# Optimization experiments

Measured on AMD Instinct MI355X. Metric: run time of the kernel, lower is better.

## Reference

```python
import jax, jax.numpy as jnp
import numpy as np

INPUT_DIM = 256
HIDDEN_DIM = 128
N = 16384


def setup_inputs() -> dict:
    key = jax.random.key(0)
    k_h, k_wq, k_bq, k_wk, k_bk = jax.random.split(key, 5)
    s = 1.0 / np.sqrt(INPUT_DIM)
    return {
        "H": jax.random.normal(k_h, (N, INPUT_DIM), dtype=jnp.float32),
        "Wq": jax.random.uniform(k_wq, (INPUT_DIM, HIDDEN_DIM), jnp.float32, -s, s),
        "bq": jax.random.uniform(k_bq, (HIDDEN_DIM,), jnp.float32, -s, s),
        "Wk": jax.random.uniform(k_wk, (INPUT_DIM, HIDDEN_DIM), jnp.float32, -s, s),
        "bk": jax.random.uniform(k_bk, (HIDDEN_DIM,), jnp.float32, -s, s),
    }


def reference(H, Wq, bq, Wk, bk):
    n = H.shape[0]
    Q = H @ Wq + bq                      # [N, hidden]
    K = H @ Wk + bk                      # [N, hidden]
    A = Q @ K.T                          # [N, N]
    # zero the diagonal BEFORE scaling/softmax (faithful to torch.where(eye,...))
    A = jnp.where(jnp.eye(n, dtype=bool), jnp.float32(0.0), A)
    A = A / jnp.sqrt(jnp.float32(K.shape[-1]))
    A = jax.nn.softmax(A, axis=-1)
    return A @ H + H                     # [N, T]
```

## Files before the change

### kernel.cpp

```cpp
#include <hip/hip_runtime.h>
#include <hip/hip_bf16.h>

#define NROWS 16384
#define DIN   256
#define DH    128
#define SPLITS 4
#define KVSPL  4096
#define KVBLK  64
#define NIT    (KVSPL / KVBLK)
#define QBLK   256

typedef __attribute__((ext_vector_type(8)))  short  short8;
typedef __attribute__((ext_vector_type(4)))  float  f32x4;
typedef __attribute__((ext_vector_type(16))) float  f32x16;
typedef __attribute__((ext_vector_type(4)))  unsigned short u16x4;
typedef __attribute__((ext_vector_type(4)))  unsigned int   u32x4;

__device__ __forceinline__ unsigned short f2bf(float f) {
  unsigned int u = __float_as_uint(f);
  unsigned int r = (u + 0x7FFFu + ((u >> 16) & 1u)) >> 16;
  return (unsigned short)r;
}
__device__ __forceinline__ float bf2f(unsigned short b) {
  return __uint_as_float(((unsigned int)b) << 16);
}

__device__ __forceinline__ void gload_lds16(const void* g, void* l) {
  __builtin_amdgcn_global_load_lds(
      (const __attribute__((address_space(1))) unsigned int*)g,
      (__attribute__((address_space(3))) unsigned int*)l, 16, 0, 0);
}

__global__ void prep_w(const float* __restrict__ Wq, const float* __restrict__ Wk,
                       unsigned short* __restrict__ WqT, unsigned short* __restrict__ WkT) {
  const float* W = blockIdx.x ? Wk : Wq;
  unsigned short* WT = blockIdx.x ? WkT : WqT;
  int c = threadIdx.x;
  for (int k = 0; k < DIN; ++k)
    WT[c * DIN + k] = f2bf(W[k * DH + c]);
}

__global__ __launch_bounds__(128) void prep_hqk(
    const float* __restrict__ H,
    const unsigned short* __restrict__ WqT, const float* __restrict__ bq,
    const unsigned short* __restrict__ WkT, const float* __restrict__ bk,
    unsigned short* __restrict__ HbT,
    unsigned short* __restrict__ Qb, unsigned short* __restrict__ Kb) {
  __shared__ __align__(16) unsigned short tile[32][264];
  const int tid = threadIdx.x;
  const int qbase = blockIdx.x * 32;

  for (int i = tid; i < 32 * 64; i += 128) {
    int r = i >> 6, c4 = i & 63;
    const f32x4 v = *reinterpret_cast<const f32x4*>(H + (size_t)(qbase + r) * DIN + c4 * 4);
    u16x4 b;
    b[0] = f2bf(v[0]); b[1] = f2bf(v[1]); b[2] = f2bf(v[2]); b[3] = f2bf(v[3]);
    *reinterpret_cast<u16x4*>(&tile[r][c4 * 4]) = b;
  }
  __syncthreads();

  for (int i = tid; i < 256 * 4; i += 128) {
    int c = i >> 2, seg = i & 3;
    short8 t;
#pragma unroll
    for (int j = 0; j < 8; ++j) t[j] = (short)tile[seg * 8 + j][c];
    *reinterpret_cast<short8*>(HbT + (size_t)c * NROWS + qbase + seg * 8) = t;
  }

  const int lane = tid & 63, w = tid >> 6;
  const int col = lane & 15, grp = lane >> 4;

  short8 ah[8];
#pragma unroll
  for (int c = 0; c < 8; ++c)
    ah[c] = *reinterpret_cast<const short8*>(&tile[w * 16 + col][c * 32 + grp * 8]);

  f32x4 accq[8], acck[8];
#pragma unroll
  for (int ct = 0; ct < 8; ++ct) { accq[ct] = f32x4{0,0,0,0}; acck[ct] = f32x4{0,0,0,0}; }

#pragma unroll
  for (int ct = 0; ct < 8; ++ct) {
#pragma unroll
    for (int c = 0; c < 8; ++c) {
      short8 bwq = *reinterpret_cast<const short8*>(WqT + (size_t)(ct * 16 + col) * DIN + c * 32 + grp * 8);
      accq[ct] = __builtin_amdgcn_mfma_f32_16x16x32_bf16(ah[c], bwq, accq[ct], 0, 0, 0);
      short8 bwk = *reinterpret_cast<const short8*>(WkT + (size_t)(ct * 16 + col) * DIN + c * 32 + grp * 8);
      acck[ct] = __builtin_amdgcn_mfma_f32_16x16x32_bf16(ah[c], bwk, acck[ct], 0, 0, 0);
    }
  }

  const float QSCALE = 0.12751742f;
#pragma unroll
  for (int ct = 0; ct < 8; ++ct) {
    float vbq = bq[ct * 16 + col];
    float vbk = bk[ct * 16 + col];
#pragma unroll
    for (int r = 0; r < 4; ++r) {
      int row = qbase + w * 16 + grp * 4 + r;
      Qb[(size_t)row * DH + ct * 16 + col] = f2bf((accq[ct][r] + vbq) * QSCALE);
      Kb[(size_t)row * DH + ct * 16 + col] = f2bf(acck[ct][r] + vbk);
    }
  }
}

__global__ __launch_bounds__(512, 2) void attn_fa(
    const unsigned short* __restrict__ Qb, const unsigned short* __restrict__ Kb,
    const unsigned short* __restrict__ HbT,
    unsigned short* __restrict__ Opart, float* __restrict__ Lp) {
  __shared__ __align__(16) char lds[99328];
  char* KtC = lds;
  char* VtC = lds + 32768;
  float* LsmF = (float*)(lds + 98304);

  const int tid = threadIdx.x;
  const int lane = tid & 63, w = tid >> 6;
  const int l31 = lane & 31, hi = lane >> 5;
  const int swz = (lane & 7) << 4;

  const int sp = blockIdx.x & 3;
  const int qb = blockIdx.x >> 2;
  const int qrow0 = qb * QBLK + w * 32;
  const int kv0 = sp * KVSPL;

  int koff[2];
#pragma unroll
  for (int s = 0; s < 2; ++s) {
    int kvl = (w * 2 + s) * 4 + (lane >> 4);
    int byt = (lane & 15) * 16;
    koff[s] = kvl * DH + ((byt ^ ((kvl & 7) << 4)) >> 1);
  }
  size_t voff[4];
#pragma unroll
  for (int s = 0; s < 4; ++s) {
    int d = (w * 4 + s) * 8 + (lane >> 3);
    int byt = (lane & 7) * 16;
    voff[s] = (size_t)d * NROWS + ((byt ^ ((d & 7) << 4)) >> 1);
  }

  short8 qf[8];
#pragma unroll
  for (int c = 0; c < 8; ++c)
    qf[c] = *reinterpret_cast<const short8*>(Qb + (size_t)(qrow0 + l31) * DH + c * 16 + hi * 8);

  f32x16 acc[8];
#pragma unroll
  for (int dt = 0; dt < 8; ++dt) acc[dt] = {};
  float lsum = 0.f;

  {
    const unsigned short* kbsrc = Kb + (size_t)kv0 * DH;
#pragma unroll
    for (int s = 0; s < 2; ++s)
      gload_lds16(kbsrc + koff[s], KtC + (w * 2 + s) * 1024);
#pragma unroll
    for (int s = 0; s < 4; ++s)
      gload_lds16(HbT + voff[s] + kv0, VtC + (w * 4 + s) * 1024);
  }

  const int dlv = l31 - 4 * hi;

  for (int it = 0; it < NIT; ++it) {
    const int pb = it & 1;
    char* Krd = KtC + pb * 16384;
    char* Vrd = VtC + pb * 32768;
    char* Kwr = KtC + (pb ^ 1) * 16384;
    char* Vwr = VtC + (pb ^ 1) * 32768;
    const int kvbase = kv0 + it * KVBLK;
    const int kvnext = kvbase + KVBLK;

    {
      const unsigned short* kbsrc = Kb + (size_t)kvnext * DH;
#pragma unroll
      for (int s = 0; s < 2; ++s)
        gload_lds16(kbsrc + koff[s], Kwr + (w * 2 + s) * 1024);
#pragma unroll
      for (int s = 0; s < 4; ++s)
        gload_lds16(HbT + voff[s] + kvnext, Vwr + (w * 4 + s) * 1024);
    }

    asm volatile("s_waitcnt vmcnt(6)" ::: "memory");
    __builtin_amdgcn_s_barrier();
    __builtin_amdgcn_sched_barrier(0);

    f32x16 p0 = {}, p1 = {};
#pragma unroll
    for (int c = 0; c < 8; ++c) {
      const int off = (c * 32 + hi * 16) ^ swz;
      short8 ka0 = *reinterpret_cast<const short8*>(Krd + l31 * 256 + off);
      short8 ka1 = *reinterpret_cast<const short8*>(Krd + 8192 + l31 * 256 + off);
      p0 = __builtin_amdgcn_mfma_f32_32x32x16_bf16(ka0, qf[c], p0, 0, 0, 0);
      p1 = __builtin_amdgcn_mfma_f32_32x32x16_bf16(ka1, qf[c], p1, 0, 0, 0);
    }

    const unsigned dq = (unsigned)(qrow0 - kvbase);
    if (dq < 64u) {
      if (dq == 0) {
#pragma unroll
        for (int r = 0; r < 16; ++r)
          if (dlv == ((r & 3) + 8 * (r >> 2))) p0[r] = 0.f;
      } else {
#pragma unroll
        for (int r = 0; r < 16; ++r)
          if (dlv == ((r & 3) + 8 * (r >> 2))) p1[r] = 0.f;
      }
    }

#pragma unroll
    for (int r = 0; r < 16; ++r) { p0[r] = exp2f(p0[r]); lsum += p0[r]; }
#pragma unroll
    for (int r = 0; r < 16; ++r) { p1[r] = exp2f(p1[r]); lsum += p1[r]; }

    unsigned int W[16];
#pragma unroll
    for (int j = 0; j < 8; ++j) {
      asm("v_cvt_pk_bf16_f32 %0, %1, %2" : "=v"(W[j])     : "v"(p0[2*j]), "v"(p0[2*j+1]));
      asm("v_cvt_pk_bf16_f32 %0, %1, %2" : "=v"(W[8 + j]) : "v"(p1[2*j]), "v"(p1[2*j+1]));
    }
#pragma unroll
    for (int b = 0; b < 4; ++b) {
      asm("v_permlane32_swap_b32 %0, %1" : "+v"(W[b*4+0]), "+v"(W[b*4+2]));
      asm("v_permlane32_swap_b32 %0, %1" : "+v"(W[b*4+1]), "+v"(W[b*4+3]));
    }

#pragma unroll
    for (int kc = 0; kc < 4; ++kc) {
      u32x4 paw = { W[kc*4+0], W[kc*4+1], W[kc*4+2], W[kc*4+3] };
      short8 pa = __builtin_bit_cast(short8, paw);
      const int off = (kc * 32 + hi * 16) ^ swz;
#pragma unroll
      for (int dt = 0; dt < 8; ++dt) {
        short8 bv = *reinterpret_cast<const short8*>(Vrd + (dt * 32 + l31) * 128 + off);
        acc[dt] = __builtin_amdgcn_mfma_f32_32x32x16_bf16(pa, bv, acc[dt], 0, 0, 0);
      }
    }

    __builtin_amdgcn_sched_barrier(0);
    __builtin_amdgcn_s_barrier();
  }

  lsum += __shfl_xor(lsum, 32);
  if (lane < 32) LsmF[w * 32 + l31] = lsum;
  asm volatile("s_waitcnt lgkmcnt(0)" ::: "memory");
  __builtin_amdgcn_sched_barrier(0);

  float rl[16];
#pragma unroll
  for (int r = 0; r < 16; ++r)
    rl[r] = 1.0f / LsmF[w * 32 + ((r & 3) + 8 * (r >> 2) + 4 * hi)];

  const size_t obase = (size_t)sp * NROWS * DIN;
#pragma unroll
  for (int dt = 0; dt < 8; ++dt) {
#pragma unroll
    for (int r = 0; r < 16; ++r) {
      int q = qrow0 + (r & 3) + 8 * (r >> 2) + 4 * hi;
      Opart[obase + (size_t)q * DIN + dt * 32 + l31] = f2bf(acc[dt][r] * rl[r]);
    }
  }
  if (lane < 32) Lp[(size_t)sp * NROWS + qrow0 + l31] = lsum;
}

__global__ __launch_bounds__(256) void merge_split(
    const unsigned short* __restrict__ Opart, const float* __restrict__ Lp,
    const float* __restrict__ H, float* __restrict__ out) {
  const int row = blockIdx.x * 16 + (threadIdx.x >> 4);
  const int d0 = (threadIdx.x & 15) * 16;

  float ls[SPLITS], Wt = 0.f;
#pragma unroll
  for (int s = 0; s < SPLITS; ++s) {
    ls[s] = Lp[(size_t)s * NROWS + row];
    Wt += ls[s];
  }
  float invW = 1.0f / Wt;

  float acc[16];
#pragma unroll
  for (int j = 0; j < 16; ++j) acc[j] = 0.f;
#pragma unroll
  for (int s = 0; s < SPLITS; ++s) {
    const unsigned short* p = Opart + ((size_t)s * NROWS + row) * DIN + d0;
#pragma unroll
    for (int h = 0; h < 2; ++h) {
      short8 v = *reinterpret_cast<const short8*>(p + h * 8);
#pragma unroll
      for (int j = 0; j < 8; ++j) acc[h * 8 + j] += ls[s] * bf2f((unsigned short)v[j]);
    }
  }
  const float* hrow = H + (size_t)row * DIN + d0;
  float* orow = out + (size_t)row * DIN + d0;
#pragma unroll
  for (int q = 0; q < 4; ++q) {
    f32x4 hv = *reinterpret_cast<const f32x4*>(hrow + q * 4);
    f32x4 ov;
#pragma unroll
    for (int j = 0; j < 4; ++j) ov[j] = acc[q * 4 + j] * invW + hv[j];
    *reinterpret_cast<f32x4*>(orow + q * 4) = ov;
  }
}

extern "C" void kernel_launch(void* const* d_in, const int* in_sizes, int n_in,
                              void* d_out, int out_size, void* d_ws, size_t ws_size,
                              hipStream_t stream) {
  const float* H  = (const float*)d_in[0];
  const float* Wq = (const float*)d_in[1];
  const float* bq = (const float*)d_in[2];
  const float* Wk = (const float*)d_in[3];
  const float* bk = (const float*)d_in[4];
  float* out = (float*)d_out;

  char* ws = (char*)d_ws;
  unsigned short* HbT   = (unsigned short*)(ws);
  unsigned short* Qb    = (unsigned short*)(ws + 8388608);
  unsigned short* Kb    = (unsigned short*)(ws + 12582912);
  unsigned short* WqT   = (unsigned short*)(ws + 16777216);
  unsigned short* WkT   = (unsigned short*)(ws + 16842752);
  unsigned short* Opart = (unsigned short*)(ws + 20971520);
  float*          Lp    = (float*)(ws + 54525952);

  prep_w<<<2, 128, 0, stream>>>(Wq, Wk, WqT, WkT);
  prep_hqk<<<512, 128, 0, stream>>>(H, WqT, bq, WkT, bk, HbT, Qb, Kb);
  attn_fa<<<256, 512, 0, stream>>>(Qb, Kb, HbT, Opart, Lp);
  merge_split<<<1024, 256, 0, stream>>>(Opart, Lp, H, out);
}
```

Measured before the change: 318.7 us.

## Load K straight to registers, 4-stage V ring, restage prep stores, drop per-split normalization

The attention kernel no longer stages K through LDS. Each wave now loads its K fragments directly from global memory into registers, and LDS becomes a 4-deep ring of V tiles with a new swizzle, with s_setprio set around the MFMA sections. The partial outputs are stored unnormalized, so the merge kernel just sums them and divides by the total sum, removing the per-split reciprocal and LDS round trip. The prep kernel doubles its rows per block and writes Q/K through LDS as coalesced 16-byte rows. The direct K loads depend on cache hits from every wave, and storing unnormalized bf16 partials changes rounding.

```diff
diff --git a/kernel.cpp b/kernel.cpp
--- a/kernel.cpp
+++ b/kernel.cpp
@@ -7,7 +7,7 @@
 #define SPLITS 4
 #define KVSPL  4096
 #define KVBLK  64
-#define NIT    (KVSPL / KVBLK)
+#define NIT    64
 #define QBLK   256
 
 typedef __attribute__((ext_vector_type(8)))  short  short8;
@@ -40,17 +40,17 @@
     WT[c * DIN + k] = f2bf(W[k * DH + c]);
 }
 
-__global__ __launch_bounds__(128) void prep_hqk(
+__global__ __launch_bounds__(256) void prep_hqk(
     const float* __restrict__ H,
     const unsigned short* __restrict__ WqT, const float* __restrict__ bq,
     const unsigned short* __restrict__ WkT, const float* __restrict__ bk,
     unsigned short* __restrict__ HbT,
     unsigned short* __restrict__ Qb, unsigned short* __restrict__ Kb) {
-  __shared__ __align__(16) unsigned short tile[32][264];
+  __shared__ __align__(16) unsigned short tile[64][264];
   const int tid = threadIdx.x;
-  const int qbase = blockIdx.x * 32;
-
-  for (int i = tid; i < 32 * 64; i += 128) {
+  const int qbase = blockIdx.x * 64;
+
+  for (int i = tid; i < 64 * 64; i += 256) {
     int r = i >> 6, c4 = i & 63;
     const f32x4 v = *reinterpret_cast<const f32x4*>(H + (size_t)(qbase + r) * DIN + c4 * 4);
     u16x4 b;
@@ -59,8 +59,8 @@
   }
   __syncthreads();
 
-  for (int i = tid; i < 256 * 4; i += 128) {
-    int c = i >> 2, seg = i & 3;
+  for (int i = tid; i < 256 * 8; i += 256) {
+    int c = i >> 3, seg = i & 7;
     short8 t;
 #pragma unroll
     for (int j = 0; j < 8; ++j) t[j] = (short)tile[seg * 8 + j][c];
@@ -91,16 +91,33 @@
   }
 
   const float QSCALE = 0.12751742f;
-#pragma unroll
-  for (int ct = 0; ct < 8; ++ct) {
-    float vbq = bq[ct * 16 + col];
-    float vbk = bk[ct * 16 + col];
-#pragma unroll
-    for (int r = 0; r < 4; ++r) {
-      int row = qbase + w * 16 + grp * 4 + r;
-      Qb[(size_t)row * DH + ct * 16 + col] = f2bf((accq[ct][r] + vbq) * QSCALE);
-      Kb[(size_t)row * DH + ct * 16 + col] = f2bf(acck[ct][r] + vbk);
-    }
+  float vbq[8], vbk[8];
+#pragma unroll
+  for (int ct = 0; ct < 8; ++ct) { vbq[ct] = bq[ct * 16 + col]; vbk[ct] = bk[ct * 16 + col]; }
+
+  __syncthreads();
+#pragma unroll
+  for (int ct = 0; ct < 8; ++ct)
+#pragma unroll
+    for (int r = 0; r < 4; ++r)
+      tile[w * 16 + grp * 4 + r][ct * 16 + col] = f2bf((accq[ct][r] + vbq[ct]) * QSCALE);
+  __syncthreads();
+  for (int i = tid; i < 1024; i += 256) {
+    int r = i >> 4, seg = i & 15;
+    *reinterpret_cast<short8*>(Qb + (size_t)(qbase + r) * DH + seg * 8) =
+        *reinterpret_cast<const short8*>(&tile[r][seg * 8]);
+  }
+  __syncthreads();
+#pragma unroll
+  for (int ct = 0; ct < 8; ++ct)
+#pragma unroll
+    for (int r = 0; r < 4; ++r)
+      tile[w * 16 + grp * 4 + r][ct * 16 + col] = f2bf(acck[ct][r] + vbk[ct]);
+  __syncthreads();
+  for (int i = tid; i < 1024; i += 256) {
+    int r = i >> 4, seg = i & 15;
+    *reinterpret_cast<short8*>(Kb + (size_t)(qbase + r) * DH + seg * 8) =
+        *reinterpret_cast<const short8*>(&tile[r][seg * 8]);
   }
 }
 
@@ -108,35 +125,26 @@
     const unsigned short* __restrict__ Qb, const unsigned short* __restrict__ Kb,
     const unsigned short* __restrict__ HbT,
     unsigned short* __restrict__ Opart, float* __restrict__ Lp) {
-  __shared__ __align__(16) char lds[99328];
-  char* KtC = lds;
-  char* VtC = lds + 32768;
-  float* LsmF = (float*)(lds + 98304);
+  __shared__ __align__(16) char lds[131072];
 
   const int tid = threadIdx.x;
   const int lane = tid & 63, w = tid >> 6;
   const int l31 = lane & 31, hi = lane >> 5;
-  const int swz = (lane & 7) << 4;
+  const int vswz = (l31 & 7) << 4;
+  const int dlv = l31 - 4 * hi;
 
   const int sp = blockIdx.x & 3;
   const int qb = blockIdx.x >> 2;
   const int qrow0 = qb * QBLK + w * 32;
   const int kv0 = sp * KVSPL;
 
-  int koff[2];
-#pragma unroll
-  for (int s = 0; s < 2; ++s) {
-    int kvl = (w * 2 + s) * 4 + (lane >> 4);
-    int byt = (lane & 15) * 16;
-    koff[s] = kvl * DH + ((byt ^ ((kvl & 7) << 4)) >> 1);
-  }
   size_t voff[4];
 #pragma unroll
   for (int s = 0; s < 4; ++s) {
-    int d = (w * 4 + s) * 8 + (lane >> 3);
-    int byt = (lane & 7) * 16;
-    voff[s] = (size_t)d * NROWS + ((byt ^ ((d & 7) << 4)) >> 1);
-  }
+    int d = w * 32 + s * 8 + (lane >> 3);
+    voff[s] = (size_t)d * NROWS + (((((lane & 7) * 16) ^ ((lane >> 3) << 4))) >> 1);
+  }
+  const int vdst = w * 4096;
 
   short8 qf[8];
 #pragma unroll
@@ -148,106 +156,93 @@
   for (int dt = 0; dt < 8; ++dt) acc[dt] = {};
   float lsum = 0.f;
 
-  {
-    const unsigned short* kbsrc = Kb + (size_t)kv0 * DH;
-#pragma unroll
-    for (int s = 0; s < 2; ++s)
-      gload_lds16(kbsrc + koff[s], KtC + (w * 2 + s) * 1024);
-#pragma unroll
-    for (int s = 0; s < 4; ++s)
-      gload_lds16(HbT + voff[s] + kv0, VtC + (w * 4 + s) * 1024);
-  }
-
-  const int dlv = l31 - 4 * hi;
-
-  for (int it = 0; it < NIT; ++it) {
-    const int pb = it & 1;
-    char* Krd = KtC + pb * 16384;
-    char* Vrd = VtC + pb * 32768;
-    char* Kwr = KtC + (pb ^ 1) * 16384;
-    char* Vwr = VtC + (pb ^ 1) * 32768;
-    const int kvbase = kv0 + it * KVBLK;
-    const int kvnext = kvbase + KVBLK;
-
-    {
-      const unsigned short* kbsrc = Kb + (size_t)kvnext * DH;
-#pragma unroll
-      for (int s = 0; s < 2; ++s)
-        gload_lds16(kbsrc + koff[s], Kwr + (w * 2 + s) * 1024);
-#pragma unroll
-      for (int s = 0; s < 4; ++s)
-        gload_lds16(HbT + voff[s] + kvnext, Vwr + (w * 4 + s) * 1024);
+#pragma unroll
+  for (int s = 0; s < 4; ++s)
+    gload_lds16(HbT + voff[s] + kv0, lds + vdst + s * 1024);
+
+  for (int ot = 0; ot < NIT / 4; ++ot) {
+#pragma unroll
+    for (int pz = 0; pz < 4; ++pz) {
+      const int it = ot * 4 + pz;
+      const int kvbase = kv0 + it * KVBLK;
+      const char* Vrd = lds + pz * 32768;
+      char* Vwr = lds + ((pz + 1) & 3) * 32768;
+
+      const unsigned short* kA = Kb + (size_t)(kvbase + l31) * DH + hi * 8;
+      const unsigned short* kB = Kb + (size_t)(kvbase + 32 + l31) * DH + hi * 8;
+      short8 ka0[8], ka1[8];
+#pragma unroll
+      for (int c = 0; c < 8; ++c) {
+        ka0[c] = *reinterpret_cast<const short8*>(kA + c * 16);
+        ka1[c] = *reinterpret_cast<const short8*>(kB + c * 16);
+      }
+
+      {
+        const size_t kvn = (size_t)kvbase + KVBLK;
+#pragma unroll
+        for (int s = 0; s < 4; ++s)
+          gload_lds16(HbT + voff[s] + kvn, Vwr + vdst + s * 1024);
+      }
+
+      asm volatile("s_waitcnt vmcnt(20)" ::: "memory");
+      __builtin_amdgcn_s_barrier();
+
+      f32x16 p0 = {}, p1 = {};
+      __builtin_amdgcn_s_setprio(1);
+#pragma unroll
+      for (int c = 0; c < 8; ++c) {
+        p0 = __builtin_amdgcn_mfma_f32_32x32x16_bf16(ka0[c], qf[c], p0, 0, 0, 0);
+        p1 = __builtin_amdgcn_mfma_f32_32x32x16_bf16(ka1[c], qf[c], p1, 0, 0, 0);
+      }
+      __builtin_amdgcn_s_setprio(0);
+
+      const unsigned dq = (unsigned)(qrow0 - kvbase);
+      if (dq < 64u) {
+        if (dq == 0) {
+#pragma unroll
+          for (int r = 0; r < 16; ++r)
+            if (dlv == ((r & 3) + 8 * (r >> 2))) p0[r] = 0.f;
+        } else {
+#pragma unroll
+          for (int r = 0; r < 16; ++r)
+            if (dlv == ((r & 3) + 8 * (r >> 2))) p1[r] = 0.f;
+        }
+      }
+
+#pragma unroll
+      for (int r = 0; r < 16; ++r) { p0[r] = exp2f(p0[r]); lsum += p0[r]; }
+#pragma unroll
+      for (int r = 0; r < 16; ++r) { p1[r] = exp2f(p1[r]); lsum += p1[r]; }
+
+      unsigned int W[16];
+#pragma unroll
+      for (int j = 0; j < 8; ++j) {
+        asm("v_cvt_pk_bf16_f32 %0, %1, %2" : "=v"(W[j])     : "v"(p0[2*j]), "v"(p0[2*j+1]));
+        asm("v_cvt_pk_bf16_f32 %0, %1, %2" : "=v"(W[8 + j]) : "v"(p1[2*j]), "v"(p1[2*j+1]));
+      }
+#pragma unroll
+      for (int b = 0; b < 4; ++b) {
+        asm("v_permlane32_swap_b32 %0, %1" : "+v"(W[b*4+0]), "+v"(W[b*4+2]));
+        asm("v_permlane32_swap_b32 %0, %1" : "+v"(W[b*4+1]), "+v"(W[b*4+3]));
+      }
+
+      __builtin_amdgcn_s_setprio(1);
+#pragma unroll
+      for (int kc = 0; kc < 4; ++kc) {
+        u32x4 paw = { W[kc*4+0], W[kc*4+1], W[kc*4+2], W[kc*4+3] };
+        short8 pa = __builtin_bit_cast(short8, paw);
+        const int off = (kc * 32 + hi * 16) ^ vswz;
+#pragma unroll
+        for (int dt = 0; dt < 8; ++dt) {
+          short8 bv = *reinterpret_cast<const short8*>(Vrd + (dt * 32 + l31) * 128 + off);
+          acc[dt] = __builtin_amdgcn_mfma_f32_32x32x16_bf16(pa, bv, acc[dt], 0, 0, 0);
+        }
+      }
+      __builtin_amdgcn_s_setprio(0);
     }
-
-    asm volatile("s_waitcnt vmcnt(6)" ::: "memory");
-    __builtin_amdgcn_s_barrier();
-    __builtin_amdgcn_sched_barrier(0);
-
-    f32x16 p0 = {}, p1 = {};
-#pragma unroll
-    for (int c = 0; c < 8; ++c) {
-      const int off = (c * 32 + hi * 16) ^ swz;
-      short8 ka0 = *reinterpret_cast<const short8*>(Krd + l31 * 256 + off);
-      short8 ka1 = *reinterpret_cast<const short8*>(Krd + 8192 + l31 * 256 + off);
-      p0 = __builtin_amdgcn_mfma_f32_32x32x16_bf16(ka0, qf[c], p0, 0, 0, 0);
-      p1 = __builtin_amdgcn_mfma_f32_32x32x16_bf16(ka1, qf[c], p1, 0, 0, 0);
-    }
-
-    const unsigned dq = (unsigned)(qrow0 - kvbase);
-    if (dq < 64u) {
-      if (dq == 0) {
-#pragma unroll
-        for (int r = 0; r < 16; ++r)
-          if (dlv == ((r & 3) + 8 * (r >> 2))) p0[r] = 0.f;
-      } else {
-#pragma unroll
-        for (int r = 0; r < 16; ++r)
-          if (dlv == ((r & 3) + 8 * (r >> 2))) p1[r] = 0.f;
-      }
-    }
-
-#pragma unroll
-    for (int r = 0; r < 16; ++r) { p0[r] = exp2f(p0[r]); lsum += p0[r]; }
-#pragma unroll
-    for (int r = 0; r < 16; ++r) { p1[r] = exp2f(p1[r]); lsum += p1[r]; }
-
-    unsigned int W[16];
-#pragma unroll
-    for (int j = 0; j < 8; ++j) {
-      asm("v_cvt_pk_bf16_f32 %0, %1, %2" : "=v"(W[j])     : "v"(p0[2*j]), "v"(p0[2*j+1]));
-      asm("v_cvt_pk_bf16_f32 %0, %1, %2" : "=v"(W[8 + j]) : "v"(p1[2*j]), "v"(p1[2*j+1]));
-    }
-#pragma unroll
-    for (int b = 0; b < 4; ++b) {
-      asm("v_permlane32_swap_b32 %0, %1" : "+v"(W[b*4+0]), "+v"(W[b*4+2]));
-      asm("v_permlane32_swap_b32 %0, %1" : "+v"(W[b*4+1]), "+v"(W[b*4+3]));
-    }
-
-#pragma unroll
-    for (int kc = 0; kc < 4; ++kc) {
-      u32x4 paw = { W[kc*4+0], W[kc*4+1], W[kc*4+2], W[kc*4+3] };
-      short8 pa = __builtin_bit_cast(short8, paw);
-      const int off = (kc * 32 + hi * 16) ^ swz;
-#pragma unroll
-      for (int dt = 0; dt < 8; ++dt) {
-        short8 bv = *reinterpret_cast<const short8*>(Vrd + (dt * 32 + l31) * 128 + off);
-        acc[dt] = __builtin_amdgcn_mfma_f32_32x32x16_bf16(pa, bv, acc[dt], 0, 0, 0);
-      }
-    }
-
-    __builtin_amdgcn_sched_barrier(0);
-    __builtin_amdgcn_s_barrier();
   }
 
   lsum += __shfl_xor(lsum, 32);
-  if (lane < 32) LsmF[w * 32 + l31] = lsum;
-  asm volatile("s_waitcnt lgkmcnt(0)" ::: "memory");
-  __builtin_amdgcn_sched_barrier(0);
-
-  float rl[16];
-#pragma unroll
-  for (int r = 0; r < 16; ++r)
-    rl[r] = 1.0f / LsmF[w * 32 + ((r & 3) + 8 * (r >> 2) + 4 * hi)];
 
   const size_t obase = (size_t)sp * NROWS * DIN;
 #pragma unroll
@@ -255,7 +250,7 @@
 #pragma unroll
     for (int r = 0; r < 16; ++r) {
       int q = qrow0 + (r & 3) + 8 * (r >> 2) + 4 * hi;
-      Opart[obase + (size_t)q * DIN + dt * 32 + l31] = f2bf(acc[dt][r] * rl[r]);
+      Opart[obase + (size_t)q * DIN + dt * 32 + l31] = f2bf(acc[dt][r]);
     }
   }
   if (lane < 32) Lp[(size_t)sp * NROWS + qrow0 + l31] = lsum;
@@ -267,12 +262,9 @@
   const int row = blockIdx.x * 16 + (threadIdx.x >> 4);
   const int d0 = (threadIdx.x & 15) * 16;
 
-  float ls[SPLITS], Wt = 0.f;
-#pragma unroll
-  for (int s = 0; s < SPLITS; ++s) {
-    ls[s] = Lp[(size_t)s * NROWS + row];
-    Wt += ls[s];
-  }
+  float Wt = 0.f;
+#pragma unroll
+  for (int s = 0; s < SPLITS; ++s) Wt += Lp[(size_t)s * NROWS + row];
   float invW = 1.0f / Wt;
 
   float acc[16];
@@ -285,7 +277,7 @@
     for (int h = 0; h < 2; ++h) {
       short8 v = *reinterpret_cast<const short8*>(p + h * 8);
 #pragma unroll
-      for (int j = 0; j < 8; ++j) acc[h * 8 + j] += ls[s] * bf2f((unsigned short)v[j]);
+      for (int j = 0; j < 8; ++j) acc[h * 8 + j] += bf2f((unsigned short)v[j]);
     }
   }
   const float* hrow = H + (size_t)row * DIN + d0;
@@ -320,7 +312,7 @@
   float*          Lp    = (float*)(ws + 54525952);
 
   prep_w<<<2, 128, 0, stream>>>(Wq, Wk, WqT, WkT);
-  prep_hqk<<<512, 128, 0, stream>>>(H, WqT, bq, WkT, bk, HbT, Qb, Kb);
+  prep_hqk<<<256, 256, 0, stream>>>(H, WqT, bq, WkT, bk, HbT, Qb, Kb);
   attn_fa<<<256, 512, 0, stream>>>(Qb, Kb, HbT, Opart, Lp);
   merge_split<<<1024, 256, 0, stream>>>(Opart, Lp, H, out);
 }
```

Result: slower. 960.4 us (+201.3%).
